# Kernel optimization log

Measured on AMD Instinct MI355X. Metric: run time of the kernel, lower is better.

## Reference

```python
import jax, jax.numpy as jnp
import numpy as np

B, N, K = 4, 4096, 16      # batch, points, knn neighbors (knn_point(16, ...))
CIN, C = 9, 128            # in_channels = 3 + extra(6); block width
NCLS = 13


def setup_inputs():
    key = jax.random.key(0)
    ks = jax.random.split(key, 16)
    def w(i, shape):
        return jax.random.normal(ks[i], shape, jnp.float32) * 0.05
    return {
        "inputs": jax.random.normal(ks[0], (B, CIN, N), jnp.float32),
        "emb_w1": w(1, (C, CIN)),
        "emb_s1": jnp.ones((C,), jnp.float32),
        "emb_b1": jnp.zeros((C,), jnp.float32),
        "emb_w2": w(2, (C, C)),
        "emb_s2": jnp.ones((C,), jnp.float32),
        "emb_b2": jnp.zeros((C,), jnp.float32),
        "blk_wq": w(3, (3, C, C)),
        "blk_wk": w(4, (3, C, C)),
        "blk_wv": w(5, (3, C, C)),
        "blk_wpos": w(6, (3, C, 3)),
        "blk_wo": w(7, (3, C, C)),
        "blk_s": jnp.ones((3, C), jnp.float32),
        "blk_b": jnp.zeros((3, C), jnp.float32),
        "fuse_w": w(8, (1024, 3 * C)),
        "fuse_s": jnp.ones((1024,), jnp.float32),
        "fuse_b": jnp.zeros((1024,), jnp.float32),
        "cls_w1": w(9, (512, 3072)),
        "cls_bias1": jnp.zeros((512,), jnp.float32),
        "cls_s1": jnp.ones((512,), jnp.float32),
        "cls_sh1": jnp.zeros((512,), jnp.float32),
        "cls_w2": w(10, (256, 512)),
        "cls_bias2": jnp.zeros((256,), jnp.float32),
        "cls_s2": jnp.ones((256,), jnp.float32),
        "cls_sh2": jnp.zeros((256,), jnp.float32),
        "cls_w3": w(11, (NCLS, 256)),
        "cls_bias3": jnp.zeros((NCLS,), jnp.float32),
    }


def reference(inputs, emb_w1, emb_s1, emb_b1, emb_w2, emb_s2, emb_b2,
              blk_wq, blk_wk, blk_wv, blk_wpos, blk_wo, blk_s, blk_b,
              fuse_w, fuse_s, fuse_b,
              cls_w1, cls_bias1, cls_s1, cls_sh1,
              cls_w2, cls_bias2, cls_s2, cls_sh2,
              cls_w3, cls_bias3):
    xyz = inputs[:, :3, :]                                    # [B,3,N]
    # --- brute-force 16-NN (knn_point): pairwise sq. distances + top-k ---
    sq = jnp.sum(xyz * xyz, axis=1)                           # [B,N]
    d = sq[:, :, None] + sq[:, None, :] - 2.0 * jnp.einsum('bcn,bcm->bnm', xyz, xyz)
    _, idx = jax.lax.top_k(-d, K)                             # [B,N,K] nearest (self incl.)
    gather = jax.vmap(lambda t, i: t[i])                      # [N,c],[N,K] -> [N,K,c]

    def cbr(x, w, s, b):                                      # Conv1d(1x1,no bias)+BN(eval)+ReLU
        return jax.nn.relu(s[None, :, None] * jnp.einsum('oc,bcn->bon', w, x) + b[None, :, None])

    x = cbr(cbr(inputs, emb_w1, emb_s1, emb_b1), emb_w2, emb_s2, emb_b2)  # [B,C,N]

    xyz_t = jnp.transpose(xyz, (0, 2, 1))                     # [B,N,3]
    rel = xyz_t[:, :, None, :] - gather(xyz_t, idx)           # [B,N,K,3] relative coords
    scale = 1.0 / jnp.sqrt(jnp.asarray(C, jnp.float32))

    xs = []
    for i in range(3):                                        # PVDSA_Res blocks (point-branch local attention)
        q = jnp.einsum('oc,bcn->bno', blk_wq[i], x)           # [B,N,C]
        k = jnp.einsum('oc,bcn->bno', blk_wk[i], x)
        v = jnp.einsum('oc,bcn->bno', blk_wv[i], x)
        k_n = gather(k, idx)                                  # [B,N,K,C]
        v_n = gather(v, idx) + jnp.einsum('oc,bnkc->bnko', blk_wpos[i], rel)
        attn = jax.nn.softmax(jnp.einsum('bnc,bnkc->bnk', q, k_n) * scale, axis=-1)
        agg = jnp.einsum('bnk,bnkc->bnc', attn, v_n)
        y = jnp.einsum('oc,bnc->bon', blk_wo[i], agg)         # out projection -> [B,C,N]
        x = x + jax.nn.relu(blk_s[i][None, :, None] * y + blk_b[i][None, :, None])  # res=True
        xs.append(x)

    x = jnp.concatenate(xs, axis=1)                           # [B,3C,N]
    x = fuse_s[None, :, None] * jnp.einsum('oc,bcn->bon', fuse_w, x) + fuse_b[None, :, None]
    x = jnp.where(x > 0, x, 0.2 * x)                          # LeakyReLU(0.2) -> [B,1024,N]

    g = jnp.concatenate([jnp.max(x, axis=-1), jnp.mean(x, axis=-1)], axis=1)  # [B,2048]
    b_, _, n_ = x.shape
    x = jnp.concatenate([x, jnp.broadcast_to(g[:, :, None], (b_, g.shape[1], n_))], axis=1)  # [B,3072,N]

    def cbbr(x, w, bias, s, sh):                              # Conv1d(1x1,bias)+BN(eval)+ReLU
        return jax.nn.relu(s[None, :, None] * (jnp.einsum('oc,bcn->bon', w, x) + bias[None, :, None]) + sh[None, :, None])

    x = cbbr(x, cls_w1, cls_bias1, cls_s1, cls_sh1)           # Dropout = identity (eval)
    x = cbbr(x, cls_w2, cls_bias2, cls_s2, cls_sh2)
    return jnp.einsum('oc,bcn->bon', cls_w3, x) + cls_bias3[None, :, None]  # [B,NCLS,N]
```

## Files before the change

kernel.cpp:

```cpp
#include <hip/hip_runtime.h>


#define NB 4
#define NP 4096
#define NT 16384

#define SCRATCH_BYTES (132u*1024u*1024u)
__device__ __align__(256) unsigned char g_scratch[SCRATCH_BYTES];

typedef __attribute__((ext_vector_type(8))) short short8;
typedef __attribute__((ext_vector_type(4))) float f32x4;
typedef __attribute__((ext_vector_type(4))) unsigned short ushort4v;

__device__ __forceinline__ float bf2f(unsigned short u){
  unsigned int v = ((unsigned int)u) << 16;
  return __builtin_bit_cast(float, v);
}
__device__ __forceinline__ unsigned short f2bf(float f){
  unsigned int x = __builtin_bit_cast(unsigned int, f);
  x += 0x7fffu + ((x >> 16) & 1u);
  return (unsigned short)(x >> 16);
}
__device__ __forceinline__ float sq3(float x, float y, float z){
  return __fadd_rn(__fadd_rn(__fmul_rn(x,x), __fmul_rn(y,y)), __fmul_rn(z,z));
}

#define KINS4(a0,a1,a2,a3,dd) do{ float _d=(dd);\
  a3=fminf(fmaxf(a2,_d),a3); a2=fminf(fmaxf(a1,_d),a2);\
  a1=fminf(fmaxf(a0,_d),a1); a0=fminf(a0,_d);}while(0)

#define KDECLD float d0=3.0e38f,d1=3.0e38f,d2=3.0e38f,d3=3.0e38f,d4=3.0e38f,\
  d5=3.0e38f,d6=3.0e38f,d7=3.0e38f,d8=3.0e38f,d9=3.0e38f,d10=3.0e38f,\
  d11=3.0e38f,d12=3.0e38f,d13=3.0e38f,d14=3.0e38f,d15=3.0e38f
#define KINSD(dd) do{ float _d=(dd); \
  d15=fminf(fmaxf(d14,_d),d15); d14=fminf(fmaxf(d13,_d),d14); \
  d13=fminf(fmaxf(d12,_d),d13); d12=fminf(fmaxf(d11,_d),d12); \
  d11=fminf(fmaxf(d10,_d),d11); d10=fminf(fmaxf(d9 ,_d),d10); \
  d9 =fminf(fmaxf(d8 ,_d),d9 ); d8 =fminf(fmaxf(d7 ,_d),d8 ); \
  d7 =fminf(fmaxf(d6 ,_d),d7 ); d6 =fminf(fmaxf(d5 ,_d),d6 ); \
  d5 =fminf(fmaxf(d4 ,_d),d5 ); d4 =fminf(fmaxf(d3 ,_d),d4 ); \
  d3 =fminf(fmaxf(d2 ,_d),d3 ); d2 =fminf(fmaxf(d1 ,_d),d2 ); \
  d1 =fminf(fmaxf(d0 ,_d),d1 ); d0 =fminf(d0,_d); }while(0)

#define KDECL KDECLD; int i0=0,i1=0,i2=0,i3=0,i4=0,i5=0,i6=0,i7=0,i8=0,\
  i9=0,i10=0,i11=0,i12=0,i13=0,i14=0,i15=0
#define KINS(dd,mm) do{ float _d=(dd); int _m=(mm); \
  bool c15 = _d < d15; \
  bool c14 = _d < d14;  i15 = c14 ? i14 : (c15 ? _m : i15);  d15 = fminf(fmaxf(d14,_d), d15); \
  bool c13 = _d < d13;  i14 = c13 ? i13 : (c14 ? _m : i14);  d14 = fminf(fmaxf(d13,_d), d14); \
  bool c12 = _d < d12;  i13 = c12 ? i12 : (c13 ? _m : i13);  d13 = fminf(fmaxf(d12,_d), d13); \
  bool c11 = _d < d11;  i12 = c11 ? i11 : (c12 ? _m : i12);  d12 = fminf(fmaxf(d11,_d), d12); \
  bool c10 = _d < d10;  i11 = c10 ? i10 : (c11 ? _m : i11);  d11 = fminf(fmaxf(d10,_d), d11); \
  bool c9  = _d < d9;   i10 = c9  ? i9  : (c10 ? _m : i10);  d10 = fminf(fmaxf(d9 ,_d), d10); \
  bool c8  = _d < d8;   i9  = c8  ? i8  : (c9  ? _m : i9 );  d9  = fminf(fmaxf(d8 ,_d), d9 ); \
  bool c7  = _d < d7;   i8  = c7  ? i7  : (c8  ? _m : i8 );  d8  = fminf(fmaxf(d7 ,_d), d8 ); \
  bool c6  = _d < d6;   i7  = c6  ? i6  : (c7  ? _m : i7 );  d7  = fminf(fmaxf(d6 ,_d), d7 ); \
  bool c5  = _d < d5;   i6  = c5  ? i5  : (c6  ? _m : i6 );  d6  = fminf(fmaxf(d5 ,_d), d6 ); \
  bool c4  = _d < d4;   i5  = c4  ? i4  : (c5  ? _m : i5 );  d5  = fminf(fmaxf(d4 ,_d), d5 ); \
  bool c3  = _d < d3;   i4  = c3  ? i3  : (c4  ? _m : i4 );  d4  = fminf(fmaxf(d3 ,_d), d4 ); \
  bool c2  = _d < d2;   i3  = c2  ? i2  : (c3  ? _m : i3 );  d3  = fminf(fmaxf(d2 ,_d), d3 ); \
  bool c1  = _d < d1;   i2  = c1  ? i1  : (c2  ? _m : i2 );  d2  = fminf(fmaxf(d1 ,_d), d2 ); \
  bool c0  = _d < d0;   i1  = c0  ? i0  : (c1  ? _m : i1 );  d1  = fminf(fmaxf(d0 ,_d), d1 ); \
  i0 = c0 ? _m : i0;  d0 = fminf(d0,_d); }while(0)

struct CvtArgs {
  const float* src[8];
  unsigned dstOff[8];
  int n[8];
};
__global__ __launch_bounds__(256) void cvt_all(CvtArgs a)
{
  int y = blockIdx.y;
  const float* src = a.src[y];
  unsigned short* dst = (unsigned short*)(g_scratch + a.dstOff[y]);
  int n = a.n[y];
  if (y == 7){
    for (int i = blockIdx.x*256 + threadIdx.x; i < n; i += gridDim.x*256){
      int r = i >> 10, c = i & 1023;
      dst[i] = f2bf(src[(size_t)r*3072 + c]);
    }
  } else {
    for (int i = blockIdx.x*256 + threadIdx.x; i < n; i += gridDim.x*256)
      dst[i] = f2bf(src[i]);
  }
}

__global__ __launch_bounds__(256) void knn_p1(const float* __restrict__ in,
                                              unsigned pdOff)
{
  float* pdist = (float*)(g_scratch + pdOff);
  __shared__ float4 sp[256];
  int b = blockIdx.z, qc = blockIdx.x, cc = blockIdx.y;
  const float* xb = in + (size_t)b*9*NP;
  int base = cc*256;
  {
    int i = threadIdx.x;
    float x = xb[base+i], y = xb[NP+base+i], z = xb[2*NP+base+i];
    sp[i] = make_float4(x,y,z, x*x+y*y+z*z);
  }
  __syncthreads();
  int n = qc*256 + threadIdx.x;
  float xn=xb[n], yn=xb[NP+n], zn=xb[2*NP+n];
  float sqn = xn*xn + yn*yn + zn*zn;
  float A0=3e38f,A1=3e38f,A2=3e38f,A3=3e38f;
  float B0=3e38f,B1=3e38f,B2=3e38f,B3=3e38f;
  float C0=3e38f,C1=3e38f,C2=3e38f,C3=3e38f;
  float D0=3e38f,D1=3e38f,D2=3e38f,D3=3e38f;
  for (int mm=0; mm<256; mm+=4){
    float4 p0 = sp[mm], p1 = sp[mm+1], p2 = sp[mm+2], p3 = sp[mm+3];
    float e0 = sqn + p0.w - 2.f*(xn*p0.x + yn*p0.y + zn*p0.z);
    float e1 = sqn + p1.w - 2.f*(xn*p1.x + yn*p1.y + zn*p1.z);
    float e2 = sqn + p2.w - 2.f*(xn*p2.x + yn*p2.y + zn*p2.z);
    float e3 = sqn + p3.w - 2.f*(xn*p3.x + yn*p3.y + zn*p3.z);
    KINS4(A0,A1,A2,A3,e0);
    KINS4(B0,B1,B2,B3,e1);
    KINS4(C0,C1,C2,C3,e2);
    KINS4(D0,D1,D2,D3,e3);
  }
  size_t ob = ((size_t)(b*16+cc)*16)*NP + n;
  pdist[ob+ 0*(size_t)NP]=A0; pdist[ob+ 1*(size_t)NP]=A1; pdist[ob+ 2*(size_t)NP]=A2; pdist[ob+ 3*(size_t)NP]=A3;
  pdist[ob+ 4*(size_t)NP]=B0; pdist[ob+ 5*(size_t)NP]=B1; pdist[ob+ 6*(size_t)NP]=B2; pdist[ob+ 7*(size_t)NP]=B3;
  pdist[ob+ 8*(size_t)NP]=C0; pdist[ob+ 9*(size_t)NP]=C1; pdist[ob+10*(size_t)NP]=C2; pdist[ob+11*(size_t)NP]=C3;
  pdist[ob+12*(size_t)NP]=D0; pdist[ob+13*(size_t)NP]=D1; pdist[ob+14*(size_t)NP]=D2; pdist[ob+15*(size_t)NP]=D3;
}

__global__ __launch_bounds__(256) void knn_thr(unsigned pdOff, unsigned thrOff)
{
  const float* pdist = (const float*)(g_scratch + pdOff);
  float* thr = (float*)(g_scratch + thrOff);
  int t = blockIdx.x*256 + threadIdx.x;
  int b = t >> 12, n = t & 4095;
  KDECLD;
  for (int cc=0; cc<16; ++cc){
    size_t ob = ((size_t)(b*16+cc)*16)*NP + n;
    #pragma unroll
    for (int j=0;j<16;j++){ KINSD(pdist[ob + (size_t)j*NP]); }
  }
  thr[t] = d15*1.000002f + 2e-4f;
}

__global__ __launch_bounds__(256) void knn_p2(const float* __restrict__ in,
                                              unsigned thrOff, unsigned pdOff, unsigned piOff)
{
  const float* thr = (const float*)(g_scratch + thrOff);
  float* pdist = (float*)(g_scratch + pdOff);
  int*   pidx  = (int*)  (g_scratch + piOff);
  __shared__ float4 sp[256];
  int b = blockIdx.z, qc = blockIdx.x, cc = blockIdx.y;
  const float* xb = in + (size_t)b*9*NP;
  int base = cc*256;
  {
    int i = threadIdx.x;
    float x = xb[base+i], y = xb[NP+base+i], z = xb[2*NP+base+i];
    sp[i] = make_float4(x,y,z,sq3(x,y,z));
  }
  __syncthreads();
  int n = qc*256 + threadIdx.x;
  float xn=xb[n], yn=xb[NP+n], zn=xb[2*NP+n];
  float sqn = sq3(xn,yn,zn);
  float th = thr[(b<<12) + n];
  size_t o = ((size_t)((b*16 + cc)*NP + n))*16;
  int cnt = 0;
  for (int mm=0; mm<256; ++mm){
    float4 p = sp[mm];
    float dot = __fadd_rn(__fadd_rn(__fmul_rn(xn,p.x), __fmul_rn(yn,p.y)), __fmul_rn(zn,p.z));
    float d = __fsub_rn(__fadd_rn(sqn, p.w), __fmul_rn(2.0f, dot));
    if (d <= th && cnt < 16){
      pdist[o+cnt] = d;
      pidx[o+cnt] = base + mm;
      cnt++;
    }
  }
  if (cnt < 16) pdist[o+cnt] = 3.0e38f;
}

__global__ __launch_bounds__(64) void knn_mrg(unsigned pdOff, unsigned piOff, unsigned idxOff)
{
  const float* pdist = (const float*)(g_scratch + pdOff);
  const int*   pidx  = (const int*)  (g_scratch + piOff);
  int*         idxOut= (int*)(g_scratch + idxOff);
  int t = blockIdx.x*64 + threadIdx.x;
  int b = t >> 12, n = t & 4095;
  KDECL;
  for (int cc=0; cc<16; ++cc){
    size_t o = ((size_t)((b*16 + cc)*NP + n))*16;
    #pragma unroll 1
    for (int j=0;j<16;j++){
      float pd = pdist[o+j];
      if (pd >= 1.0e38f) break;
      KINS(pd, pidx[o+j]);
    }
  }
  idxOut[t*16+ 0]=i0;  idxOut[t*16+ 1]=i1;  idxOut[t*16+ 2]=i2;  idxOut[t*16+ 3]=i3;
  idxOut[t*16+ 4]=i4;  idxOut[t*16+ 5]=i5;  idxOut[t*16+ 6]=i6;  idxOut[t*16+ 7]=i7;
  idxOut[t*16+ 8]=i8;  idxOut[t*16+ 9]=i9;  idxOut[t*16+10]=i10; idxOut[t*16+11]=i11;
  idxOut[t*16+12]=i12; idxOut[t*16+13]=i13; idxOut[t*16+14]=i14; idxOut[t*16+15]=i15;
}

__global__ __launch_bounds__(256) void emb1_kernel(const float* __restrict__ in,
                                                   const float* __restrict__ w1,
                                                   const float* __restrict__ s1,
                                                   const float* __restrict__ b1,
                                                   unsigned x1Off)
{
  unsigned short* x1 = (unsigned short*)(g_scratch + x1Off);
  int og = blockIdx.y*32;
  __shared__ float wf[32*9], sf[32], bf_[32];
  for (int i = threadIdx.x; i < 32*9; i += 256) wf[i] = w1[og*9 + i];
  if (threadIdx.x < 32){ sf[threadIdx.x]=s1[og+threadIdx.x]; bf_[threadIdx.x]=b1[og+threadIdx.x]; }
  __syncthreads();
  int t = blockIdx.x*256 + threadIdx.x;
  int b = t >> 12, n = t & 4095;
  float v[9];
  #pragma unroll
  for (int c=0;c<9;c++) v[c] = in[((size_t)b*9 + c)*NP + n];
  for (int o=0;o<32;o+=2){
    float a0=0.f, a1=0.f;
    #pragma unroll
    for (int c=0;c<9;c++){ a0 += wf[o*9+c]*v[c]; a1 += wf[(o+1)*9+c]*v[c]; }
    a0 = fmaxf(sf[o]*a0 + bf_[o], 0.f);
    a1 = fmaxf(sf[o+1]*a1 + bf_[o+1], 0.f);
    unsigned pk = (unsigned)f2bf(a0) | ((unsigned)f2bf(a1) << 16);
    *(unsigned*)(x1 + (size_t)t*128 + og + o) = pk;
  }
}

enum { EPI_PLAIN=0, EPI_RELU_SB=1, EPI_RES=2, EPI_LEAKY=3, EPI_CLS=4 };

template<int EPI, bool EXB>
__device__ __forceinline__ void gemm_body(
    int M0, int T0,
    const unsigned short* W, const unsigned short* X, unsigned short* out,
    int Xstride, int Xoff, int outStride, int outOff,
    const float* sPtr, const float* bPtr,
    const float* extraIn, unsigned extraOffB, int extraStride,
    unsigned resOffB, int resStride, int resOff,
    int K, int Astride, int lane)
{
  int r = lane & 15, q = lane >> 4;
  f32x4 acc[4][4];
  #pragma unroll
  for (int i=0;i<4;i++)
    #pragma unroll
    for (int j=0;j<4;j++)
      #pragma unroll
      for (int u=0;u<4;u++) acc[i][j][u] = 0.f;

  const unsigned short* Arow[4]; const unsigned short* Brow[4];
  #pragma unroll
  for (int i=0;i<4;i++) Arow[i] = W + (size_t)(M0 + i*16 + r)*Astride + q*8;
  #pragma unroll
  for (int j=0;j<4;j++) Brow[j] = X + (size_t)(T0 + j*16 + r)*Xstride + Xoff + q*8;

  short8 a[4], bfr[4];
  #pragma unroll
  for (int i=0;i<4;i++) a[i]   = *(const short8*)(Arow[i]);
  #pragma unroll
  for (int j=0;j<4;j++) bfr[j] = *(const short8*)(Brow[j]);
  for (int k0=32; k0<K; k0+=32){
    short8 a2[4], b2[4];
    #pragma unroll
    for (int i=0;i<4;i++) a2[i] = *(const short8*)(Arow[i] + k0);
    #pragma unroll
    for (int j=0;j<4;j++) b2[j] = *(const short8*)(Brow[j] + k0);
    #pragma unroll
    for (int i=0;i<4;i++)
      #pragma unroll
      for (int j=0;j<4;j++)
        acc[i][j] = __builtin_amdgcn_mfma_f32_16x16x32_bf16(a[i], bfr[j], acc[i][j], 0, 0, 0);
    #pragma unroll
    for (int i=0;i<4;i++) a[i] = a2[i];
    #pragma unroll
    for (int j=0;j<4;j++) bfr[j] = b2[j];
  }
  #pragma unroll
  for (int i=0;i<4;i++)
    #pragma unroll
    for (int j=0;j<4;j++)
      acc[i][j] = __builtin_amdgcn_mfma_f32_16x16x32_bf16(a[i], bfr[j], acc[i][j], 0, 0, 0);

  #pragma unroll
  for (int i=0;i<4;i++){
    int m = M0 + i*16 + q*4;
    float sv[4], bv[4];
    if constexpr (EPI != EPI_PLAIN){
      #pragma unroll
      for (int u=0;u<4;u++){ sv[u]=sPtr[m+u]; bv[u]=bPtr[m+u]; }
    }
    #pragma unroll
    for (int j=0;j<4;j++){
      int token = T0 + j*16 + r;
      float ex[4];
      if constexpr (EPI == EPI_CLS){
        int bb = token >> 12;
        #pragma unroll
        for (int u=0;u<4;u++)
          ex[u] = EXB ? extraIn[bb*extraStride + m + u]
                      : ((const float*)(g_scratch + extraOffB))[bb*extraStride + m + u];
      }
      float resv[4];
      if constexpr (EPI == EPI_RES){
        const unsigned short* resPtr = (const unsigned short*)(g_scratch + resOffB);
        ushort4v rv = *(const ushort4v*)(resPtr + (size_t)token*resStride + resOff + m);
        #pragma unroll
        for (int u=0;u<4;u++) resv[u]=bf2f(rv[u]);
      }
      ushort4v ov;
      #pragma unroll
      for (int u=0;u<4;u++){
        float aa = acc[i][j][u];
        float vo;
        if constexpr (EPI == EPI_PLAIN)        vo = aa;
        else if constexpr (EPI == EPI_RELU_SB) vo = fmaxf(sv[u]*aa + bv[u], 0.f);
        else if constexpr (EPI == EPI_RES)     vo = resv[u] + fmaxf(sv[u]*aa + bv[u], 0.f);
        else if constexpr (EPI == EPI_LEAKY){  float tt = sv[u]*aa + bv[u]; vo = tt>0.f ? tt : 0.2f*tt; }
        else { vo = fmaxf(sv[u]*(aa + ex[u]) + bv[u], 0.f); }
        ov[u] = f2bf(vo);
      }
      *(ushort4v*)(out + (size_t)token*outStride + outOff + m) = ov;
    }
  }
}

template<int EPI, bool EXB>
__global__ __launch_bounds__(256) void gemm_tok(
    unsigned W0off, unsigned W1off, unsigned W2off,
    unsigned O0off, unsigned O1off, unsigned O2off,
    unsigned XoffB, int Xstride, int Xoff,
    int outStride, int outOff,
    const float* sPtr, const float* bPtr,
    const float* extraIn, unsigned extraOffB, int extraStride,
    unsigned resOffB, int resStride, int resOff,
    int K, int Astride)
{
  const unsigned short* X = (const unsigned short*)(g_scratch + XoffB);
  unsigned wOffB   = (blockIdx.z==0) ? W0off : ((blockIdx.z==1) ? W1off : W2off);
  unsigned outOffB = (blockIdx.z==0) ? O0off : ((blockIdx.z==1) ? O1off : O2off);
  const unsigned short* W = (const unsigned short*)(g_scratch + wOffB);
  unsigned short* out = (unsigned short*)(g_scratch + outOffB);
  int lin = blockIdx.x + gridDim.x*blockIdx.y;
  int bx = lin >> 7;
  int by = (lin & 7)*16 + ((lin >> 3) & 15);
  int lane = threadIdx.x & 63, wave = threadIdx.x >> 6;
  int M0 = bx*128 + (wave>>1)*64;
  int T0 = by*128 + (wave&1)*64;
  gemm_body<EPI,EXB>(M0, T0, W, X, out, Xstride, Xoff, outStride, outOff,
                     sPtr, bPtr, extraIn, extraOffB, extraStride,
                     resOffB, resStride, resOff, K, Astride, lane);
}

template<int EPI, bool EXB>
__global__ __launch_bounds__(128) void gemm_small(
    unsigned W0off, unsigned W1off, unsigned W2off,
    unsigned O0off, unsigned O1off, unsigned O2off,
    unsigned XoffB, int Xstride, int Xoff,
    int outStride, int outOff,
    const float* sPtr, const float* bPtr,
    const float* extraIn, unsigned extraOffB, int extraStride,
    unsigned resOffB, int resStride, int resOff,
    int K, int Astride)
{
  const unsigned short* X = (const unsigned short*)(g_scratch + XoffB);
  unsigned wOffB   = (blockIdx.z==0) ? W0off : ((blockIdx.z==1) ? W1off : W2off);
  unsigned outOffB = (blockIdx.z==0) ? O0off : ((blockIdx.z==1) ? O1off : O2off);
  const unsigned short* W = (const unsigned short*)(g_scratch + wOffB);
  unsigned short* out = (unsigned short*)(g_scratch + outOffB);
  int lane = threadIdx.x & 63, wave = threadIdx.x >> 6;
  int M0 = blockIdx.x*64;
  int T0 = blockIdx.y*128 + wave*64;
  gemm_body<EPI,EXB>(M0, T0, W, X, out, Xstride, Xoff, outStride, outOff,
                     sPtr, bPtr, extraIn, extraOffB, extraStride,
                     resOffB, resStride, resOff, K, Astride, lane);
}

__global__ __launch_bounds__(256) void attn_kernel(
  unsigned qOff, unsigned kOff, unsigned vOff, unsigned idxOff,
  const float* __restrict__ in, const float* __restrict__ wpos,
  unsigned aggOff)
{
  const unsigned short* Q  = (const unsigned short*)(g_scratch + qOff);
  const unsigned short* Kf = (const unsigned short*)(g_scratch + kOff);
  const unsigned short* V  = (const unsigned short*)(g_scratch + vOff);
  const int* idx           = (const int*)(g_scratch + idxOff);
  unsigned short* agg      = (unsigned short*)(g_scratch + aggOff);

  int lane = threadIdx.x & 63, wv = threadIdx.x >> 6;
  int t = blockIdx.x*4 + wv;
  int b = t >> 12, n = t & 4095;
  const float* xb = in + (size_t)b*9*NP;
  int c0 = lane*2;

  unsigned qv = *(const unsigned*)(Q + (size_t)t*128 + c0);
  float q0 = bf2f((unsigned short)(qv & 0xffff)), q1 = bf2f((unsigned short)(qv >> 16));
  float xn = xb[n], yn = xb[NP+n], zn = xb[2*NP+n];
  float wp00=wpos[c0*3+0],     wp01=wpos[c0*3+1],     wp02=wpos[c0*3+2];
  float wp10=wpos[(c0+1)*3+0], wp11=wpos[(c0+1)*3+1], wp12=wpos[(c0+1)*3+2];

  int mi[16]; float s[16];
  #pragma unroll
  for (int j=0;j<16;j++) mi[j] = idx[(size_t)t*16 + j] & 4095;
  #pragma unroll
  for (int j=0;j<16;j++){
    unsigned kv = *(const unsigned*)(Kf + ((size_t)(b<<12) + mi[j])*128 + c0);
    float p = q0*bf2f((unsigned short)(kv & 0xffff)) + q1*bf2f((unsigned short)(kv >> 16));
    #pragma unroll
    for (int o=32;o>=1;o>>=1) p += __shfl_xor(p, o, 64);
    s[j] = p;
  }
  const float scale = 0.08838834764831845f;
  float mx = s[0];
  #pragma unroll
  for (int j=1;j<16;j++) mx = fmaxf(mx, s[j]);
  float e[16], sum = 0.f;
  #pragma unroll
  for (int j=0;j<16;j++){ e[j] = __expf((s[j]-mx)*scale); sum += e[j]; }
  float inv = 1.f / sum;

  float a0=0.f, a1=0.f;
  #pragma unroll
  for (int j=0;j<16;j++){
    int m = mi[j];
    float w = e[j]*inv;
    unsigned vv = *(const unsigned*)(V + ((size_t)(b<<12) + m)*128 + c0);
    float rx = xn - xb[m];
    float ry = yn - xb[NP+m];
    float rz = zn - xb[2*NP+m];
    float p0 = wp00*rx + wp01*ry + wp02*rz;
    float p1 = wp10*rx + wp11*ry + wp12*rz;
    a0 += w*(bf2f((unsigned short)(vv & 0xffff)) + p0);
    a1 += w*(bf2f((unsigned short)(vv >> 16)) + p1);
  }
  unsigned pk = (unsigned)f2bf(a0) | ((unsigned)f2bf(a1) << 16);
  *(unsigned*)(agg + (size_t)t*128 + c0) = pk;
}

__global__ __launch_bounds__(256) void pool_part(unsigned xfOff, unsigned gpOff)
{
  const unsigned short* xf = (const unsigned short*)(g_scratch + xfOff);
  float* gp = (float*)(g_scratch + gpOff);
  int b = blockIdx.x >> 7, cblk = (blockIdx.x >> 3) & 15, seg = blockIdx.x & 7;
  int cl = threadIdx.x & 63, tg = threadIdx.x >> 6;
  int c = cblk*64 + cl;
  float mx = -3.0e38f, sm = 0.f;
  for (int n = seg*512 + tg; n < (seg+1)*512; n += 4){
    float v = bf2f(xf[((size_t)(b<<12) + n)*1024 + c]);
    mx = fmaxf(mx, v); sm += v;
  }
  __shared__ float smx[4][64], ssm[4][64];
  smx[tg][cl]=mx; ssm[tg][cl]=sm;
  __syncthreads();
  if (tg==0){
    #pragma unroll
    for (int k=1;k<4;k++){ mx = fmaxf(mx, smx[k][cl]); sm += ssm[k][cl]; }
    gp[((b*8 + seg)*2 + 0)*1024 + c] = mx;
    gp[((b*8 + seg)*2 + 1)*1024 + c] = sm;
  }
}
__global__ __launch_bounds__(256) void pool_final(unsigned gpOff, unsigned gOff)
{
  const float* gp = (const float*)(g_scratch + gpOff);
  float* g = (float*)(g_scratch + gOff);
  int b = blockIdx.x;
  for (int c = threadIdx.x; c < 1024; c += 256){
    float mx = -3.0e38f, sm = 0.f;
    #pragma unroll
    for (int seg=0; seg<8; ++seg){
      mx = fmaxf(mx, gp[((b*8 + seg)*2 + 0)*1024 + c]);
      sm += gp[((b*8 + seg)*2 + 1)*1024 + c];
    }
    g[b*2048 + c] = mx;
    g[b*2048 + 1024 + c] = sm * (1.f/4096.f);
  }
}

__global__ __launch_bounds__(256) void gterm_kernel(const float* __restrict__ w1,
                                                    const float* __restrict__ bias1,
                                                    unsigned gOff, unsigned gbOff)
{
  const float* g = (const float*)(g_scratch + gOff);
  float* gb = (float*)(g_scratch + gbOff);
  int b = blockIdx.x >> 3, og = (blockIdx.x & 7)*64;
  int ol = threadIdx.x & 63, cq = threadIdx.x >> 6;
  int o = og + ol;
  const float* wrow = w1 + (size_t)o*3072 + 1024 + cq*512;
  const float* gp = g + b*2048 + cq*512;
  float acc = 0.f;
  for (int c=0;c<512;c+=4){
    float4 wv4 = *(const float4*)(wrow + c);
    acc += wv4.x*gp[c] + wv4.y*gp[c+1] + wv4.z*gp[c+2] + wv4.w*gp[c+3];
  }
  __shared__ float sred[4][64];
  sred[cq][ol] = acc;
  __syncthreads();
  if (cq==0){
    acc += sred[1][ol] + sred[2][ol] + sred[3][ol];
    gb[b*512 + o] = acc + bias1[o];
  }
}

__global__ __launch_bounds__(256) void cls3_kernel(unsigned c2Off,
                                                   const float* __restrict__ w3,
                                                   const float* __restrict__ bias3,
                                                   float* __restrict__ outp)
{
  const unsigned short* c2 = (const unsigned short*)(g_scratch + c2Off);
  __shared__ float wf[13*256];
  __shared__ float bf3[13];
  for (int i=threadIdx.x;i<13*256;i+=256) wf[i]=w3[i];
  if (threadIdx.x < 13) bf3[threadIdx.x]=bias3[threadIdx.x];
  __syncthreads();
  int lane = threadIdx.x & 63, wv = threadIdx.x >> 6;
  int tl = lane >> 2, cq = lane & 3;
  int t = blockIdx.x*64 + wv*16 + tl;
  const unsigned short* xrow = c2 + (size_t)t*256 + cq*64;
  float acc[13];
  #pragma unroll
  for (int o=0;o<13;o++) acc[o]=0.f;
  for (int c=0;c<64;c+=8){
    short8 xv = *(const short8*)(xrow + c);
    float xs[8];
    #pragma unroll
    for (int u=0;u<8;u++) xs[u]=bf2f((unsigned short)xv[u]);
    #pragma unroll
    for (int o=0;o<13;o++){
      const float* wr = wf + o*256 + cq*64 + c;
      #pragma unroll
      for (int u=0;u<8;u++) acc[o] += wr[u]*xs[u];
    }
  }
  #pragma unroll
  for (int o=0;o<13;o++){
    acc[o] += __shfl_xor(acc[o], 1, 64);
    acc[o] += __shfl_xor(acc[o], 2, 64);
  }
  if (cq==0){
    int b = t >> 12, n = t & 4095;
    #pragma unroll
    for (int o=0;o<13;o++)
      outp[((size_t)b*13 + o)*NP + n] = acc[o] + bf3[o];
  }
}

extern "C" void kernel_launch(void* const* d_in, const int* in_sizes, int n_in,
                              void* d_out, int out_size, void* d_ws, size_t ws_size,
                              hipStream_t stream) {
  (void)in_sizes; (void)n_in; (void)out_size; (void)d_ws; (void)ws_size;
  const float* in      = (const float*)d_in[0];
  const float* emb_w1  = (const float*)d_in[1];
  const float* emb_s1  = (const float*)d_in[2];
  const float* emb_b1  = (const float*)d_in[3];
  const float* emb_w2  = (const float*)d_in[4];
  const float* emb_s2  = (const float*)d_in[5];
  const float* emb_b2  = (const float*)d_in[6];
  const float* blk_wq  = (const float*)d_in[7];
  const float* blk_wk  = (const float*)d_in[8];
  const float* blk_wv  = (const float*)d_in[9];
  const float* blk_wpos= (const float*)d_in[10];
  const float* blk_wo  = (const float*)d_in[11];
  const float* blk_s   = (const float*)d_in[12];
  const float* blk_b   = (const float*)d_in[13];
  const float* fuse_w  = (const float*)d_in[14];
  const float* fuse_s  = (const float*)d_in[15];
  const float* fuse_b  = (const float*)d_in[16];
  const float* cls_w1  = (const float*)d_in[17];
  const float* cls_b1  = (const float*)d_in[18];
  const float* cls_s1  = (const float*)d_in[19];
  const float* cls_sh1 = (const float*)d_in[20];
  const float* cls_w2  = (const float*)d_in[21];
  const float* cls_b2  = (const float*)d_in[22];
  const float* cls_s2  = (const float*)d_in[23];
  const float* cls_sh2 = (const float*)d_in[24];
  const float* cls_w3  = (const float*)d_in[25];
  const float* cls_b3  = (const float*)d_in[26];

  const unsigned MB = 1u<<20, KB = 1024u;
  const unsigned OFF_IDX   = 0;
  const unsigned OFF_WQ    = 1*MB;
  const unsigned OFF_WK    = 1*MB + 128*KB;
  const unsigned OFF_WV    = 1*MB + 256*KB;
  const unsigned OFF_WO    = 1*MB + 384*KB;
  const unsigned OFF_WEMB2 = 1*MB + 512*KB;
  const unsigned OFF_WFUSE = 1*MB + 576*KB;
  const unsigned OFF_WW1   = 3*MB;
  const unsigned OFF_WW2   = 4*MB;
  const unsigned OFF_X1    = 5*MB;
  const unsigned OFF_X0    = 9*MB;
  const unsigned OFF_XCAT  = 13*MB;
  const unsigned OFF_QB    = 25*MB;
  const unsigned OFF_KB    = 29*MB;
  const unsigned OFF_VB    = 33*MB;
  const unsigned OFF_AGG   = 37*MB;
  const unsigned OFF_XF    = 41*MB;
  const unsigned OFF_C1    = 73*MB;
  const unsigned OFF_C2    = 89*MB;
  const unsigned OFF_G     = 97*MB;
  const unsigned OFF_GB    = 97*MB + 64*KB;
  const unsigned OFF_GP    = 97*MB + 128*KB;
  const unsigned OFF_THR   = 97*MB + 512*KB;
  const unsigned OFF_PD    = 98*MB;
  const unsigned OFF_PI    = 114*MB;
  float* outp = (float*)d_out;

  CvtArgs ca;
  ca.src[0]=emb_w2;  ca.dstOff[0]=OFF_WEMB2; ca.n[0]=128*128;
  ca.src[1]=blk_wq;  ca.dstOff[1]=OFF_WQ;    ca.n[1]=3*128*128;
  ca.src[2]=blk_wk;  ca.dstOff[2]=OFF_WK;    ca.n[2]=3*128*128;
  ca.src[3]=blk_wv;  ca.dstOff[3]=OFF_WV;    ca.n[3]=3*128*128;
  ca.src[4]=blk_wo;  ca.dstOff[4]=OFF_WO;    ca.n[4]=3*128*128;
  ca.src[5]=fuse_w;  ca.dstOff[5]=OFF_WFUSE; ca.n[5]=1024*384;
  ca.src[6]=cls_w2;  ca.dstOff[6]=OFF_WW2;   ca.n[6]=256*512;
  ca.src[7]=cls_w1;  ca.dstOff[7]=OFF_WW1;   ca.n[7]=512*1024;
  cvt_all<<<dim3(64,8), 256, 0, stream>>>(ca);

  knn_p1<<<dim3(16,16,4), 256, 0, stream>>>(in, OFF_PD);
  knn_thr<<<dim3(64), 256, 0, stream>>>(OFF_PD, OFF_THR);
  knn_p2<<<dim3(16,16,4), 256, 0, stream>>>(in, OFF_THR, OFF_PD, OFF_PI);
  knn_mrg<<<dim3(256), 64, 0, stream>>>(OFF_PD, OFF_PI, OFF_IDX);
  emb1_kernel<<<dim3(64,4), 256, 0, stream>>>(in, emb_w1, emb_s1, emb_b1, OFF_X1);
  gemm_small<EPI_RELU_SB,false><<<dim3(2,128,1), 128, 0, stream>>>(
      OFF_WEMB2, OFF_WEMB2, OFF_WEMB2, OFF_X0, OFF_X0, OFF_X0,
      OFF_X1, 128, 0, 128, 0, emb_s2, emb_b2,
      nullptr, 0, 0, 0, 0, 0, 128, 128);
  for (int i=0;i<3;i++){
    unsigned wq = OFF_WQ + i*32768, wk = OFF_WK + i*32768;
    unsigned wv = OFF_WV + i*32768, wo = OFF_WO + i*32768;
    const float* wp = blk_wpos + i*128*3;
    const float* si = blk_s + i*128;
    const float* bi = blk_b + i*128;
    unsigned XiOff = (i==0) ? OFF_X0 : OFF_XCAT;
    int Xs = (i==0) ? 128 : 384;
    int Xo = (i==0) ? 0 : (i-1)*128;
    gemm_small<EPI_PLAIN,false><<<dim3(2,128,3), 128, 0, stream>>>(
        wq, wk, wv, OFF_QB, OFF_KB, OFF_VB,
        XiOff, Xs, Xo, 128, 0, nullptr, nullptr,
        nullptr, 0, 0, 0, 0, 0, 128, 128);
    attn_kernel<<<dim3(4096), 256, 0, stream>>>(OFF_QB, OFF_KB, OFF_VB, OFF_IDX, in, wp, OFF_AGG);
    gemm_small<EPI_RES,false><<<dim3(2,128,1), 128, 0, stream>>>(
        wo, wo, wo, OFF_XCAT, OFF_XCAT, OFF_XCAT,
        OFF_AGG, 128, 0, 384, i*128, si, bi,
        nullptr, 0, 0, XiOff, Xs, Xo, 128, 128);
  }
  gemm_tok<EPI_LEAKY,false><<<dim3(8,128,1), 256, 0, stream>>>(
      OFF_WFUSE, OFF_WFUSE, OFF_WFUSE, OFF_XF, OFF_XF, OFF_XF,
      OFF_XCAT, 384, 0, 1024, 0, fuse_s, fuse_b,
      nullptr, 0, 0, 0, 0, 0, 384, 384);
  pool_part<<<dim3(512), 256, 0, stream>>>(OFF_XF, OFF_GP);
  pool_final<<<dim3(4), 256, 0, stream>>>(OFF_GP, OFF_G);
  gterm_kernel<<<dim3(32), 256, 0, stream>>>(cls_w1, cls_b1, OFF_G, OFF_GB);
  gemm_tok<EPI_CLS,false><<<dim3(4,128,1), 256, 0, stream>>>(
      OFF_WW1, OFF_WW1, OFF_WW1, OFF_C1, OFF_C1, OFF_C1,
      OFF_XF, 1024, 0, 512, 0, cls_s1, cls_sh1,
      nullptr, OFF_GB, 512, 0, 0, 0, 1024, 1024);
  gemm_small<EPI_CLS,true><<<dim3(4,128,1), 128, 0, stream>>>(
      OFF_WW2, OFF_WW2, OFF_WW2, OFF_C2, OFF_C2, OFF_C2,
      OFF_C1, 512, 0, 256, 0, cls_s2, cls_sh2,
      cls_b2, 0, 0, 0, 0, 0, 512, 512);
  cls3_kernel<<<dim3(256), 256, 0, stream>>>(OFF_C2, cls_w3, cls_b3, outp);
}
```

Before: 601.7 us.

## Stage GEMM tiles through LDS shared across waves for large GEMMs

Replaces the per-wave direct-global-load GEMM for the fuse and classifier GEMMs with a 128x128 block tile staged in shared memory, so the four waves share A and B fragments instead of each loading its own. The cls2 GEMM moves from the small 64-row kernel to this LDS kernel with a grid of 2 by 128. The small-GEMM kernel also drops its register double-buffered prefetch in favour of a simple loop. The cost is two barriers per K step with no LDS double buffering, so global latency is exposed more directly.

```diff
diff --git a/kernel.cpp b/kernel.cpp
--- a/kernel.cpp
+++ b/kernel.cpp
@@ -228,57 +228,13 @@
 enum { EPI_PLAIN=0, EPI_RELU_SB=1, EPI_RES=2, EPI_LEAKY=3, EPI_CLS=4 };
 
 template<int EPI, bool EXB>
-__device__ __forceinline__ void gemm_body(
-    int M0, int T0,
-    const unsigned short* W, const unsigned short* X, unsigned short* out,
-    int Xstride, int Xoff, int outStride, int outOff,
+__device__ __forceinline__ void gemm_epi(
+    f32x4 (&acc)[4][4], int M0, int T0, int r, int q,
+    unsigned short* out, int outStride, int outOff,
     const float* sPtr, const float* bPtr,
     const float* extraIn, unsigned extraOffB, int extraStride,
-    unsigned resOffB, int resStride, int resOff,
-    int K, int Astride, int lane)
-{
-  int r = lane & 15, q = lane >> 4;
-  f32x4 acc[4][4];
-  #pragma unroll
-  for (int i=0;i<4;i++)
-    #pragma unroll
-    for (int j=0;j<4;j++)
-      #pragma unroll
-      for (int u=0;u<4;u++) acc[i][j][u] = 0.f;
-
-  const unsigned short* Arow[4]; const unsigned short* Brow[4];
-  #pragma unroll
-  for (int i=0;i<4;i++) Arow[i] = W + (size_t)(M0 + i*16 + r)*Astride + q*8;
-  #pragma unroll
-  for (int j=0;j<4;j++) Brow[j] = X + (size_t)(T0 + j*16 + r)*Xstride + Xoff + q*8;
-
-  short8 a[4], bfr[4];
-  #pragma unroll
-  for (int i=0;i<4;i++) a[i]   = *(const short8*)(Arow[i]);
-  #pragma unroll
-  for (int j=0;j<4;j++) bfr[j] = *(const short8*)(Brow[j]);
-  for (int k0=32; k0<K; k0+=32){
-    short8 a2[4], b2[4];
-    #pragma unroll
-    for (int i=0;i<4;i++) a2[i] = *(const short8*)(Arow[i] + k0);
-    #pragma unroll
-    for (int j=0;j<4;j++) b2[j] = *(const short8*)(Brow[j] + k0);
-    #pragma unroll
-    for (int i=0;i<4;i++)
-      #pragma unroll
-      for (int j=0;j<4;j++)
-        acc[i][j] = __builtin_amdgcn_mfma_f32_16x16x32_bf16(a[i], bfr[j], acc[i][j], 0, 0, 0);
-    #pragma unroll
-    for (int i=0;i<4;i++) a[i] = a2[i];
-    #pragma unroll
-    for (int j=0;j<4;j++) bfr[j] = b2[j];
-  }
-  #pragma unroll
-  for (int i=0;i<4;i++)
-    #pragma unroll
-    for (int j=0;j<4;j++)
-      acc[i][j] = __builtin_amdgcn_mfma_f32_16x16x32_bf16(a[i], bfr[j], acc[i][j], 0, 0, 0);
-
+    unsigned resOffB, int resStride, int resOff)
+{
   #pragma unroll
   for (int i=0;i<4;i++){
     int m = M0 + i*16 + q*4;
@@ -323,7 +279,7 @@
 }
 
 template<int EPI, bool EXB>
-__global__ __launch_bounds__(256) void gemm_tok(
+__global__ __launch_bounds__(256) void gemm_lds(
     unsigned W0off, unsigned W1off, unsigned W2off,
     unsigned O0off, unsigned O1off, unsigned O2off,
     unsigned XoffB, int Xstride, int Xoff,
@@ -333,6 +289,8 @@
     unsigned resOffB, int resStride, int resOff,
     int K, int Astride)
 {
+  __shared__ unsigned short As[128*32];
+  __shared__ unsigned short Bs[128*32];
   const unsigned short* X = (const unsigned short*)(g_scratch + XoffB);
   unsigned wOffB   = (blockIdx.z==0) ? W0off : ((blockIdx.z==1) ? W1off : W2off);
   unsigned outOffB = (blockIdx.z==0) ? O0off : ((blockIdx.z==1) ? O1off : O2off);
@@ -341,12 +299,53 @@
   int lin = blockIdx.x + gridDim.x*blockIdx.y;
   int bx = lin >> 7;
   int by = (lin & 7)*16 + ((lin >> 3) & 15);
-  int lane = threadIdx.x & 63, wave = threadIdx.x >> 6;
-  int M0 = bx*128 + (wave>>1)*64;
-  int T0 = by*128 + (wave&1)*64;
-  gemm_body<EPI,EXB>(M0, T0, W, X, out, Xstride, Xoff, outStride, outOff,
-                     sPtr, bPtr, extraIn, extraOffB, extraStride,
-                     resOffB, resStride, resOff, K, Astride, lane);
+  int M0 = bx*128, T0 = by*128;
+  int t = threadIdx.x;
+  int lane = t & 63, wave = t >> 6;
+  int r = lane & 15, q = lane >> 4;
+  int srow = t >> 2, schunk = t & 3;
+
+  const unsigned short* Ag0 = W + (size_t)(M0 + srow)*Astride + schunk*8;
+  const unsigned short* Ag1 = W + (size_t)(M0 + 64 + srow)*Astride + schunk*8;
+  const unsigned short* Bg0 = X + (size_t)(T0 + srow)*Xstride + Xoff + schunk*8;
+  const unsigned short* Bg1 = X + (size_t)(T0 + 64 + srow)*Xstride + Xoff + schunk*8;
+  unsigned short* Aw0 = &As[srow*32 + schunk*8];
+  unsigned short* Aw1 = &As[(64 + srow)*32 + schunk*8];
+  unsigned short* Bw0 = &Bs[srow*32 + schunk*8];
+  unsigned short* Bw1 = &Bs[(64 + srow)*32 + schunk*8];
+
+  int Mw = (wave>>1)*64, Tw = (wave&1)*64;
+  f32x4 acc[4][4];
+  #pragma unroll
+  for (int i=0;i<4;i++)
+    #pragma unroll
+    for (int j=0;j<4;j++)
+      #pragma unroll
+      for (int u=0;u<4;u++) acc[i][j][u] = 0.f;
+
+  for (int k0=0; k0<K; k0+=32){
+    short8 va0 = *(const short8*)(Ag0 + k0);
+    short8 va1 = *(const short8*)(Ag1 + k0);
+    short8 vb0 = *(const short8*)(Bg0 + k0);
+    short8 vb1 = *(const short8*)(Bg1 + k0);
+    if (k0) __syncthreads();
+    *(short8*)Aw0 = va0; *(short8*)Aw1 = va1;
+    *(short8*)Bw0 = vb0; *(short8*)Bw1 = vb1;
+    __syncthreads();
+    short8 a[4], bfr[4];
+    #pragma unroll
+    for (int i=0;i<4;i++) a[i]   = *(const short8*)(&As[(Mw + i*16 + r)*32 + q*8]);
+    #pragma unroll
+    for (int j=0;j<4;j++) bfr[j] = *(const short8*)(&Bs[(Tw + j*16 + r)*32 + q*8]);
+    #pragma unroll
+    for (int i=0;i<4;i++)
+      #pragma unroll
+      for (int j=0;j<4;j++)
+        acc[i][j] = __builtin_amdgcn_mfma_f32_16x16x32_bf16(a[i], bfr[j], acc[i][j], 0, 0, 0);
+  }
+  gemm_epi<EPI,EXB>(acc, M0+Mw, T0+Tw, r, q, out, outStride, outOff,
+                    sPtr, bPtr, extraIn, extraOffB, extraStride,
+                    resOffB, resStride, resOff);
 }
 
 template<int EPI, bool EXB>
@@ -366,11 +365,39 @@
   const unsigned short* W = (const unsigned short*)(g_scratch + wOffB);
   unsigned short* out = (unsigned short*)(g_scratch + outOffB);
   int lane = threadIdx.x & 63, wave = threadIdx.x >> 6;
+  int r = lane & 15, q = lane >> 4;
   int M0 = blockIdx.x*64;
   int T0 = blockIdx.y*128 + wave*64;
-  gemm_body<EPI,EXB>(M0, T0, W, X, out, Xstride, Xoff, outStride, outOff,
-                     sPtr, bPtr, extraIn, extraOffB, extraStride,
-                     resOffB, resStride, resOff, K, Astride, lane);
+
+  f32x4 acc[4][4];
+  #pragma unroll
+  for (int i=0;i<4;i++)
+    #pragma unroll
+    for (int j=0;j<4;j++)
+      #pragma unroll
+      for (int u=0;u<4;u++) acc[i][j][u] = 0.f;
+
+  const unsigned short* Arow[4]; const unsigned short* Brow[4];
+  #pragma unroll
+  for (int i=0;i<4;i++) Arow[i] = W + (size_t)(M0 + i*16 + r)*Astride + q*8;
+  #pragma unroll
+  for (int j=0;j<4;j++) Brow[j] = X + (size_t)(T0 + j*16 + r)*Xstride + Xoff + q*8;
+
+  for (int k0=0; k0<K; k0+=32){
+    short8 a[4], bfr[4];
+    #pragma unroll
+    for (int i=0;i<4;i++) a[i]   = *(const short8*)(Arow[i] + k0);
+    #pragma unroll
+    for (int j=0;j<4;j++) bfr[j] = *(const short8*)(Brow[j] + k0);
+    #pragma unroll
+    for (int i=0;i<4;i++)
+      #pragma unroll
+      for (int j=0;j<4;j++)
+        acc[i][j] = __builtin_amdgcn_mfma_f32_16x16x32_bf16(a[i], bfr[j], acc[i][j], 0, 0, 0);
+  }
+  gemm_epi<EPI,EXB>(acc, M0, T0, r, q, out, outStride, outOff,
+                    sPtr, bPtr, extraIn, extraOffB, extraStride,
+                    resOffB, resStride, resOff);
 }
 
 __global__ __launch_bounds__(256) void attn_kernel(
@@ -640,18 +667,18 @@
         OFF_AGG, 128, 0, 384, i*128, si, bi,
         nullptr, 0, 0, XiOff, Xs, Xo, 128, 128);
   }
-  gemm_tok<EPI_LEAKY,false><<<dim3(8,128,1), 256, 0, stream>>>(
+  gemm_lds<EPI_LEAKY,false><<<dim3(8,128,1), 256, 0, stream>>>(
       OFF_WFUSE, OFF_WFUSE, OFF_WFUSE, OFF_XF, OFF_XF, OFF_XF,
       OFF_XCAT, 384, 0, 1024, 0, fuse_s, fuse_b,
       nullptr, 0, 0, 0, 0, 0, 384, 384);
   pool_part<<<dim3(512), 256, 0, stream>>>(OFF_XF, OFF_GP);
   pool_final<<<dim3(4), 256, 0, stream>>>(OFF_GP, OFF_G);
   gterm_kernel<<<dim3(32), 256, 0, stream>>>(cls_w1, cls_b1, OFF_G, OFF_GB);
-  gemm_tok<EPI_CLS,false><<<dim3(4,128,1), 256, 0, stream>>>(
+  gemm_lds<EPI_CLS,false><<<dim3(4,128,1), 256, 0, stream>>>(
       OFF_WW1, OFF_WW1, OFF_WW1, OFF_C1, OFF_C1, OFF_C1,
       OFF_XF, 1024, 0, 512, 0, cls_s1, cls_sh1,
       nullptr, OFF_GB, 512, 0, 0, 0, 1024, 1024);
-  gemm_small<EPI_CLS,true><<<dim3(4,128,1), 128, 0, stream>>>(
+  gemm_lds<EPI_CLS,true><<<dim3(2,128,1), 256, 0, stream>>>(
       OFF_WW2, OFF_WW2, OFF_WW2, OFF_C2, OFF_C2, OFF_C2,
       OFF_C1, 512, 0, 256, 0, cls_s2, cls_sh2,
       cls_b2, 0, 0, 0, 0, 0, 512, 512);
```

Result: faster. 541.4 us (-10.0%).
